# Kernel tuning notes

Hardware: AMD Instinct MI355X
Metric: run time of the kernel (lower is better)

The kernel has to match this reference:

```python
import jax, jax.numpy as jnp
import numpy as np

N = 8192
IN_DIM = 64
OUT_DIM = 64
HEADS = 2
EPS = 1e-10


def setup_inputs() -> dict:
    key = jax.random.key(0)
    ks = jax.random.split(key, 6)
    features = jax.random.normal(ks[0], (N, IN_DIM), dtype=jnp.float32)
    adj = (jax.random.uniform(ks[1], (N, N)) < 0.005).astype(jnp.float32)
    # per-head attention linear: Linear(2*in_dim, 1) stacked -> [heads, 2*in_dim]
    W_attn = jax.random.normal(ks[2], (HEADS, 2 * IN_DIM), dtype=jnp.float32) * 0.05
    b_attn = jax.random.normal(ks[3], (HEADS,), dtype=jnp.float32) * 0.05
    # feature transform: Linear(in_dim, heads*out_dim)
    W_lin = jax.random.normal(ks[4], (HEADS * OUT_DIM, IN_DIM), dtype=jnp.float32) * 0.05
    b_lin = jax.random.normal(ks[5], (HEADS * OUT_DIM,), dtype=jnp.float32) * 0.05
    return {"adj": adj, "features": features, "W_attn": W_attn,
            "b_attn": b_attn, "W_lin": W_lin, "b_lin": b_lin}


def reference(adj, features, W_attn, b_attn, W_lin, b_lin):
    n, in_dim = features.shape
    heads = W_attn.shape[0]
    # add self-loops (adj + sparse identity in the original)
    idx = jnp.arange(n)
    adj_sl = adj.at[idx, idx].add(1.0)
    # concat-based score: head([x_i ; x_j]) = x_i @ Wa_src + x_j @ Wa_dst + b
    # (avoids the O(N^2 * 2*in_dim) concat tensor the original materializes)
    s_src = features @ W_attn[:, :in_dim].T   # [N, H]
    s_dst = features @ W_attn[:, in_dim:].T   # [N, H]
    # scores[n,h,m] = exp(s_src[n,h] + s_dst[m,h] + b[h])
    scores = jnp.exp(s_src[:, :, None] + s_dst.T[None, :, :] + b_attn[None, :, None])
    scores = scores * adj_sl[:, None, :]                      # adjacency mask
    attn = scores / (jnp.sum(scores, axis=-1, keepdims=True) + EPS)
    # dropout is identity in eval mode (deterministic reference)
    ft = (features @ W_lin.T + b_lin).reshape(n, heads, -1)   # [N, H, OUT]
    out = jnp.einsum('nhm,mhj->nhj', attn, ft)                # aggregate neighbors
    return jax.nn.elu(out.reshape(n, -1))
```

## Files before the change

### kernel.cpp

```cpp
#include <hip/hip_runtime.h>
#include <math.h>

#define NN 8192
#define IN_DIM 64
#define GAT_EPS 1e-10f
#define ECAP 256

typedef float fvec4 __attribute__((ext_vector_type(4)));

__device__ __forceinline__ unsigned nz4(fvec4 v) {
    return (unsigned)(v.x != 0.f) | ((unsigned)(v.y != 0.f) << 1) |
           ((unsigned)(v.z != 0.f) << 2) | ((unsigned)(v.w != 0.f) << 3);
}

__global__ void pdv_kernel(const float* __restrict__ features,
                           const float* __restrict__ W_attn,
                           float2* __restrict__ pdv) {
    int n = blockIdx.x * blockDim.x + threadIdx.x;
    const float4* f4   = (const float4*)(features + (size_t)n * IN_DIM);
    const float4* wa0d = (const float4*)(W_attn + IN_DIM);
    const float4* wa1d = (const float4*)(W_attn + 3 * IN_DIM);
    float s0 = 0.f, s1 = 0.f;
#pragma unroll
    for (int d = 0; d < IN_DIM / 4; ++d) {
        float4 f = f4[d];
        float4 b = wa0d[d];
        float4 e = wa1d[d];
        s0 += f.x * b.x + f.y * b.y + f.z * b.z + f.w * b.w;
        s1 += f.x * e.x + f.y * e.y + f.z * e.z + f.w * e.w;
    }
    pdv[n] = make_float2(__expf(s0), __expf(s1));
}

__global__ void __launch_bounds__(256) gat_agg_kernel(
        const float* __restrict__ adj,
        const float* __restrict__ features,
        const float2* __restrict__ pdv,
        const float* __restrict__ W_lin,
        const float* __restrict__ b_lin,
        float* __restrict__ out) {
    __shared__ int edges[4][ECAP];
    __shared__ int ecnt[4];
    __shared__ float aggbuf[4][2][64];
    int widx = threadIdx.x >> 6;
    int lane = threadIdx.x & 63;
    int n = blockIdx.x * 4 + widx;
    int* ebuf = edges[widx];

    if (lane == 0) ecnt[widx] = 0;

    const fvec4* arow = (const fvec4*)(adj + (size_t)n * NN) + lane;

    fvec4 q[3][4];
#pragma unroll
    for (int r = 0; r < 3; ++r) {
        const fvec4* p = arow + r * 256;
        q[r][0] = __builtin_nontemporal_load(p);
        q[r][1] = __builtin_nontemporal_load(p + 64);
        q[r][2] = __builtin_nontemporal_load(p + 128);
        q[r][3] = __builtin_nontemporal_load(p + 192);
    }

#pragma unroll
    for (int it = 0; it < 8; ++it) {
        int slot = it % 3;
        fvec4 a0 = q[slot][0], a1 = q[slot][1], a2 = q[slot][2], a3 = q[slot][3];
        if (it < 5) {
            const fvec4* p = arow + (it + 3) * 256;
            q[slot][0] = __builtin_nontemporal_load(p);
            q[slot][1] = __builtin_nontemporal_load(p + 64);
            q[slot][2] = __builtin_nontemporal_load(p + 128);
            q[slot][3] = __builtin_nontemporal_load(p + 192);
        }
        unsigned mb = nz4(a0) | (nz4(a1) << 4) | (nz4(a2) << 8) | (nz4(a3) << 12);
        if (mb) {
            int c = __popc(mb);
            int pos = atomicAdd(&ecnt[widx], c);
            int megabase = it * 1024 + lane * 4;
            while (mb) {
                int b = __ffs(mb) - 1;
                mb &= mb - 1;
                ebuf[pos++] = megabase + ((b >> 2) << 8) + (b & 3);
            }
        }
    }

    float2 ps = pdv[n];
    float fs = features[(size_t)n * 64 + lane];
    float acc0 = ps.x * fs, acc1 = ps.y * fs;
    float den0 = ps.x, den1 = ps.y;

    __syncthreads();

    int count = ecnt[widx];
    int e = 0;
    for (; e + 8 <= count; e += 8) {
        int4 ma  = *(const int4*)&ebuf[e];
        int4 mbq = *(const int4*)&ebuf[e + 4];
        float2 p0 = pdv[ma.x],  p1 = pdv[ma.y],  p2 = pdv[ma.z],  p3 = pdv[ma.w];
        float2 p4 = pdv[mbq.x], p5 = pdv[mbq.y], p6 = pdv[mbq.z], p7 = pdv[mbq.w];
        float f0 = features[(size_t)ma.x * 64 + lane];
        float f1 = features[(size_t)ma.y * 64 + lane];
        float f2 = features[(size_t)ma.z * 64 + lane];
        float f3 = features[(size_t)ma.w * 64 + lane];
        float f4v = features[(size_t)mbq.x * 64 + lane];
        float f5 = features[(size_t)mbq.y * 64 + lane];
        float f6 = features[(size_t)mbq.z * 64 + lane];
        float f7 = features[(size_t)mbq.w * 64 + lane];
        acc0 += p0.x * f0 + p1.x * f1 + p2.x * f2 + p3.x * f3
              + p4.x * f4v + p5.x * f5 + p6.x * f6 + p7.x * f7;
        acc1 += p0.y * f0 + p1.y * f1 + p2.y * f2 + p3.y * f3
              + p4.y * f4v + p5.y * f5 + p6.y * f6 + p7.y * f7;
        den0 += p0.x + p1.x + p2.x + p3.x + p4.x + p5.x + p6.x + p7.x;
        den1 += p0.y + p1.y + p2.y + p3.y + p4.y + p5.y + p6.y + p7.y;
    }
    for (; e < count; ++e) {
        int m = ebuf[e];
        float2 p = pdv[m];
        float f = features[(size_t)m * 64 + lane];
        acc0 += p.x * f;
        acc1 += p.y * f;
        den0 += p.x;
        den1 += p.y;
    }

    aggbuf[widx][0][lane] = acc0 / (den0 + GAT_EPS);
    aggbuf[widx][1][lane] = acc1 / (den1 + GAT_EPS);
    __syncthreads();

    const float4* w0 = (const float4*)(W_lin + (size_t)lane * IN_DIM);
    const float4* w1 = (const float4*)(W_lin + (size_t)(64 + lane) * IN_DIM);
    const float4* a0p = (const float4*)aggbuf[widx][0];
    const float4* a1p = (const float4*)aggbuf[widx][1];
    float o0 = 0.f, o1 = 0.f;
#pragma unroll
    for (int d = 0; d < IN_DIM / 4; ++d) {
        float4 u = w0[d];
        float4 x = a0p[d];
        float4 v = w1[d];
        float4 y = a1p[d];
        o0 += u.x * x.x + u.y * x.y + u.z * x.z + u.w * x.w;
        o1 += v.x * y.x + v.y * y.y + v.z * y.z + v.w * y.w;
    }
    o0 += b_lin[lane];
    o1 += b_lin[64 + lane];
    o0 = o0 > 0.f ? o0 : expm1f(o0);
    o1 = o1 > 0.f ? o1 : expm1f(o1);
    out[(size_t)n * 128 + lane]      = o0;
    out[(size_t)n * 128 + 64 + lane] = o1;
}

extern "C" void kernel_launch(void* const* d_in, const int* in_sizes, int n_in,
                              void* d_out, int out_size, void* d_ws, size_t ws_size,
                              hipStream_t stream) {
    const float* adj      = (const float*)d_in[0];
    const float* features = (const float*)d_in[1];
    const float* W_attn   = (const float*)d_in[2];
    const float* W_lin    = (const float*)d_in[4];
    const float* b_lin    = (const float*)d_in[5];
    float* out = (float*)d_out;

    float2* pdv = (float2*)d_ws;

    pdv_kernel<<<32, 256, 0, stream>>>(features, W_attn, pdv);
    gat_agg_kernel<<<NN / 4, 256, 0, stream>>>(adj, features, pdv, W_lin, b_lin, out);
}
```

Baseline: 374.7 us.

## Fuse per-node score computation into aggregation kernel with wave shuffles

Removes the separate pdv kernel and recomputes each neighbor's destination score inside the aggregation loop, using a 64-lane shuffle reduction over the already-loaded feature column. This drops one kernel launch and the workspace round trip. Block-wide __syncthreads are replaced by compiler memory barriers, since each wave uses only its own shared slices. The trade is extra shuffle and exp work per edge, about 12 shuffle steps per neighbor, and correctness now relies on intra-wave ordering for the LDS atomics and buffers.

```diff
diff --git a/kernel.cpp b/kernel.cpp
--- a/kernel.cpp
+++ b/kernel.cpp
@@ -13,29 +13,21 @@
            ((unsigned)(v.z != 0.f) << 2) | ((unsigned)(v.w != 0.f) << 3);
 }
 
-__global__ void pdv_kernel(const float* __restrict__ features,
-                           const float* __restrict__ W_attn,
-                           float2* __restrict__ pdv) {
-    int n = blockIdx.x * blockDim.x + threadIdx.x;
-    const float4* f4   = (const float4*)(features + (size_t)n * IN_DIM);
-    const float4* wa0d = (const float4*)(W_attn + IN_DIM);
-    const float4* wa1d = (const float4*)(W_attn + 3 * IN_DIM);
-    float s0 = 0.f, s1 = 0.f;
+__device__ __forceinline__ float2 edge_score(float f, float w0, float w1) {
+    float t0 = f * w0;
+    float t1 = f * w1;
 #pragma unroll
-    for (int d = 0; d < IN_DIM / 4; ++d) {
-        float4 f = f4[d];
-        float4 b = wa0d[d];
-        float4 e = wa1d[d];
-        s0 += f.x * b.x + f.y * b.y + f.z * b.z + f.w * b.w;
-        s1 += f.x * e.x + f.y * e.y + f.z * e.z + f.w * e.w;
+    for (int m = 32; m; m >>= 1) {
+        t0 += __shfl_xor(t0, m, 64);
+        t1 += __shfl_xor(t1, m, 64);
     }
-    pdv[n] = make_float2(__expf(s0), __expf(s1));
+    return make_float2(__expf(t0), __expf(t1));
 }
 
 __global__ void __launch_bounds__(256) gat_agg_kernel(
         const float* __restrict__ adj,
         const float* __restrict__ features,
-        const float2* __restrict__ pdv,
+        const float* __restrict__ W_attn,
         const float* __restrict__ W_lin,
         const float* __restrict__ b_lin,
         float* __restrict__ out) {
@@ -48,6 +40,9 @@
     int* ebuf = edges[widx];
 
     if (lane == 0) ecnt[widx] = 0;
+
+    float w0 = W_attn[IN_DIM + lane];
+    float w1 = W_attn[3 * IN_DIM + lane];
 
     const fvec4* arow = (const fvec4*)(adj + (size_t)n * NN) + lane;
 
@@ -85,20 +80,18 @@
         }
     }
 
-    float2 ps = pdv[n];
     float fs = features[(size_t)n * 64 + lane];
+    float2 ps = edge_score(fs, w0, w1);
     float acc0 = ps.x * fs, acc1 = ps.y * fs;
     float den0 = ps.x, den1 = ps.y;
 
-    __syncthreads();
+    asm volatile("" ::: "memory");
 
     int count = ecnt[widx];
     int e = 0;
     for (; e + 8 <= count; e += 8) {
         int4 ma  = *(const int4*)&ebuf[e];
         int4 mbq = *(const int4*)&ebuf[e + 4];
-        float2 p0 = pdv[ma.x],  p1 = pdv[ma.y],  p2 = pdv[ma.z],  p3 = pdv[ma.w];
-        float2 p4 = pdv[mbq.x], p5 = pdv[mbq.y], p6 = pdv[mbq.z], p7 = pdv[mbq.w];
         float f0 = features[(size_t)ma.x * 64 + lane];
         float f1 = features[(size_t)ma.y * 64 + lane];
         float f2 = features[(size_t)ma.z * 64 + lane];
@@ -107,6 +100,14 @@
         float f5 = features[(size_t)mbq.y * 64 + lane];
         float f6 = features[(size_t)mbq.z * 64 + lane];
         float f7 = features[(size_t)mbq.w * 64 + lane];
+        float2 p0 = edge_score(f0, w0, w1);
+        float2 p1 = edge_score(f1, w0, w1);
+        float2 p2 = edge_score(f2, w0, w1);
+        float2 p3 = edge_score(f3, w0, w1);
+        float2 p4 = edge_score(f4v, w0, w1);
+        float2 p5 = edge_score(f5, w0, w1);
+        float2 p6 = edge_score(f6, w0, w1);
+        float2 p7 = edge_score(f7, w0, w1);
         acc0 += p0.x * f0 + p1.x * f1 + p2.x * f2 + p3.x * f3
               + p4.x * f4v + p5.x * f5 + p6.x * f6 + p7.x * f7;
         acc1 += p0.y * f0 + p1.y * f1 + p2.y * f2 + p3.y * f3
@@ -116,8 +117,8 @@
     }
     for (; e < count; ++e) {
         int m = ebuf[e];
-        float2 p = pdv[m];
         float f = features[(size_t)m * 64 + lane];
+        float2 p = edge_score(f, w0, w1);
         acc0 += p.x * f;
         acc1 += p.y * f;
         den0 += p.x;
@@ -126,18 +127,18 @@
 
     aggbuf[widx][0][lane] = acc0 / (den0 + GAT_EPS);
     aggbuf[widx][1][lane] = acc1 / (den1 + GAT_EPS);
-    __syncthreads();
+    asm volatile("" ::: "memory");
 
-    const float4* w0 = (const float4*)(W_lin + (size_t)lane * IN_DIM);
-    const float4* w1 = (const float4*)(W_lin + (size_t)(64 + lane) * IN_DIM);
+    const float4* wl0 = (const float4*)(W_lin + (size_t)lane * IN_DIM);
+    const float4* wl1 = (const float4*)(W_lin + (size_t)(64 + lane) * IN_DIM);
     const float4* a0p = (const float4*)aggbuf[widx][0];
     const float4* a1p = (const float4*)aggbuf[widx][1];
     float o0 = 0.f, o1 = 0.f;
 #pragma unroll
     for (int d = 0; d < IN_DIM / 4; ++d) {
-        float4 u = w0[d];
+        float4 u = wl0[d];
         float4 x = a0p[d];
-        float4 v = w1[d];
+        float4 v = wl1[d];
         float4 y = a1p[d];
         o0 += u.x * x.x + u.y * x.y + u.z * x.z + u.w * x.w;
         o1 += v.x * y.x + v.y * y.y + v.z * y.z + v.w * y.w;
@@ -159,9 +160,7 @@
     const float* W_lin    = (const float*)d_in[4];
     const float* b_lin    = (const float*)d_in[5];
     float* out = (float*)d_out;
+    (void)d_ws; (void)ws_size;
 
-    float2* pdv = (float2*)d_ws;
-
-    pdv_kernel<<<32, 256, 0, stream>>>(features, W_attn, pdv);
-    gat_agg_kernel<<<NN / 4, 256, 0, stream>>>(adj, features, pdv, W_lin, b_lin, out);
+    gat_agg_kernel<<<NN / 4, 256, 0, stream>>>(adj, features, W_attn, W_lin, b_lin, out);
 }
```

After: 382.8 us. +2.2%, slower.
